# Performance work log

Hardware: AMD Instinct MI355X
Metric: run time of the kernel (lower is better)

## Reference

```python
import jax, jax.numpy as jnp
import numpy as np

V, NJ, NB, NP, NK = 6890, 24, 10, 207, 19
PARENTS = [-1,0,0,0,1,2,3,4,5,6,7,8,9,9,9,12,13,14,16,17,18,19,20,21]


def setup_inputs() -> dict:
    key = jax.random.key(0)
    ks = jax.random.split(key, 9)
    N = 2048
    return {
        "beta": jax.random.normal(ks[0], (N, NB), jnp.float32),
        "theta": jax.random.normal(ks[1], (N, NJ, 3), jnp.float32) * 0.2,
        "trans": jax.random.normal(ks[2], (N, 3), jnp.float32),
        "shapedirs": jax.random.normal(ks[3], (V, 3, NB), jnp.float32) * 0.03,
        "v_template": jax.random.normal(ks[4], (V, 3), jnp.float32),
        "J_regressor": jax.random.uniform(ks[5], (NJ, V), jnp.float32) / V,
        "posedirs": jax.random.normal(ks[6], (V, 3, NP), jnp.float32) * 0.01,
        "weights": jax.nn.softmax(jax.random.normal(ks[7], (V, NJ), jnp.float32) * 4.0, axis=-1),
        "joint_regressor": jax.random.uniform(ks[8], (V, NK), jnp.float32) / V,
    }


def rodrigues(r):
    # r: [M,3] axis-angle -> [M,3,3] rotation matrices
    theta = jnp.maximum(jnp.linalg.norm(r, axis=-1, keepdims=True),
                        jnp.finfo(r.dtype).tiny)  # [M,1]
    rh = r / theta
    c = jnp.cos(theta)[:, :, None]  # [M,1,1]
    s = jnp.sin(theta)[:, :, None]
    z = jnp.zeros_like(rh[:, 0])
    K = jnp.stack([z, -rh[:, 2], rh[:, 1],
                   rh[:, 2], z, -rh[:, 0],
                   -rh[:, 1], rh[:, 0], z], axis=1).reshape(-1, 3, 3)
    outer = rh[:, :, None] * rh[:, None, :]
    return c * jnp.eye(3, dtype=r.dtype) + (1.0 - c) * outer + s * K


def reference(beta, theta, trans, shapedirs, v_template, J_regressor, posedirs, weights, joint_regressor):
    N = beta.shape[0]
    dt = beta.dtype
    v_shaped = jnp.einsum('nb,vcb->nvc', beta, shapedirs) + v_template  # [N,V,3]
    J = jnp.einsum('jv,nvc->njc', J_regressor, v_shaped)                # [N,24,3]
    # pose rotations and pose blendshapes
    R = rodrigues(theta.reshape(-1, 3)).reshape(N, NJ, 3, 3)
    lrotmin = (R[:, 1:] - jnp.eye(3, dtype=dt)).reshape(N, NP)
    v_posed = v_shaped + jnp.einsum('np,vcp->nvc', lrotmin, posedirs)
    # kinematic chain: 24 small 4x4 transforms with parent dependencies
    bottom = jnp.broadcast_to(jnp.array([0., 0., 0., 1.], dtype=dt), (N, 1, 4))
    def make_A(Ri, t):  # [N,3,3],[N,3] -> [N,4,4]
        return jnp.concatenate([jnp.concatenate([Ri, t[:, :, None]], axis=2), bottom], axis=1)
    G = [make_A(R[:, 0], J[:, 0])]
    for i in range(1, NJ):
        p = PARENTS[i]
        G.append(G[p] @ make_A(R[:, i], J[:, i] - J[:, p]))
    G = jnp.stack(G, axis=1)  # [N,24,4,4]
    # subtract rest-pose joint contribution
    Jh = jnp.concatenate([J, jnp.zeros((N, NJ, 1), dt)], axis=2)[..., None]  # [N,24,4,1]
    corr = G @ Jh
    G_rel = G - jnp.concatenate([jnp.zeros((N, NJ, 4, 3), dt), corr], axis=3)
    # linear blend skinning
    T = jnp.einsum('njab,vj->nvab', G_rel, weights)  # [N,V,4,4]
    vh = jnp.concatenate([v_posed, jnp.ones((N, V, 1), dt)], axis=2)  # [N,V,4]
    v = jnp.einsum('nvab,nvb->nva', T, vh)[..., :3]
    verts = v + trans[:, None, :]
    joints = jnp.einsum('nvc,vk->nkc', verts, joint_regressor)  # [N,19,3]
    return verts, joints
```

## Files before the change

kernel.cpp:

```cpp
#include <hip/hip_runtime.h>

#define V      6890
#define NJ     24
#define NB     10
#define NP     207
#define NK     19
#define NBATCH 2048
#define KP     224
#define KC     217
#define VC     (V*3)
#define VCP    20736
#define BN     32
#define BV     64
#define VST4   260
#define VSEG   1723
#define KSTEPS 648
#define JSP    18
#define JCH    9

using bh8   = __attribute__((ext_vector_type(8))) short;
using u16x4 = __attribute__((ext_vector_type(4))) unsigned short;
using f32x4 = __attribute__((ext_vector_type(4))) float;

__constant__ int PAR[NJ] = {-1,0,0,0,1,2,3,4,5,6,7,8,9,9,9,12,13,14,16,17,18,19,20,21};

__device__ __forceinline__ unsigned short f2bf(float f) {
    unsigned int u = __float_as_uint(f);
    u += 0x7FFFu + ((u >> 16) & 1u);
    return (unsigned short)(u >> 16);
}
__device__ __forceinline__ float bf2f(unsigned short h) {
    return __uint_as_float((unsigned int)h << 16);
}

__global__ __launch_bounds__(256) void k_prep(const float* __restrict__ Jreg,
                                              const float* __restrict__ vtmpl,
                                              const float* __restrict__ sdirs,
                                              const float* __restrict__ pdirs,
                                              const float* __restrict__ jreg,
                                              float* __restrict__ JB,
                                              unsigned short* __restrict__ Bmat,
                                              unsigned short* __restrict__ JbigT) {
    int blk = blockIdx.x, tid = threadIdx.x;
    if (blk < 792) {
        int vs = blk & 3, og = blk >> 2;
        int o = og*4 + (tid >> 6);
        int lane = tid & 63;
        int j = o/33, t = o%33, c = t/11, m = t%11;
        int lo = vs*VSEG + lane, hi = min(V, vs*VSEG + VSEG);
        const float* jr = Jreg + j*V;
        float s = 0.f;
        if (m == 0) { for (int v = lo; v < hi; v += 64) s += jr[v] * vtmpl[v*3 + c]; }
        else        { for (int v = lo; v < hi; v += 64) s += jr[v] * sdirs[(v*3 + c)*NB + (m-1)]; }
        #pragma unroll
        for (int d = 1; d < 64; d <<= 1) s += __shfl_xor(s, d);
        if (lane == 0) atomicAdd(&JB[(j*3 + c)*11 + m], s);
    } else if (blk < 792 + 18144) {
        int gid = (blk - 792)*256 + tid;
        int vc = gid / KP, k = gid - vc*KP;
        float val;
        if (vc >= VC)     val = 0.f;
        else if (k < NB)  val = sdirs[vc*NB + k];
        else if (k < KC)  val = pdirs[vc*NP + (k - NB)];
        else if (k == KC) val = vtmpl[vc];
        else              val = 0.f;
        Bmat[((size_t)(k >> 5)*VCP + vc)*32 + (k & 31)] = f2bf(val);
    } else {
        int gid = (blk - 792 - 18144)*256 + tid;
        int kc = gid / VCP, vc = gid - kc*VCP;
        float val = 0.f;
        if (kc < NK*3 && vc < VC && (kc % 3) == (vc % 3))
            val = jreg[(vc/3)*NK + (kc/3)];
        JbigT[((size_t)(vc >> 5)*64 + kc)*32 + (vc & 31)] = f2bf(val);
    }
}

__global__ __launch_bounds__(64) void k_pern(const float* __restrict__ beta,
                                             const float* __restrict__ theta,
                                             const float* __restrict__ trans,
                                             const float* __restrict__ JB,
                                             unsigned short* __restrict__ Arow,
                                             unsigned short* __restrict__ Gt) {
    int n = blockIdx.x, tid = threadIdx.x;
    __shared__ float Rsm[NJ][9];
    __shared__ float Jsm[NJ][3];
    __shared__ float Gsm[NJ][12];

    if (tid < NJ) {
        const float* th = theta + (n*NJ + tid)*3;
        float x = th[0], y = th[1], z = th[2];
        float nrm = sqrtf(x*x + y*y + z*z);
        float t = fmaxf(nrm, 1.1754944e-38f);
        float inv = 1.0f / t;
        float rx = x*inv, ry = y*inv, rz = z*inv;
        float c = cosf(t), s = sinf(t), oc = 1.0f - c;
        Rsm[tid][0] = c + oc*rx*rx;      Rsm[tid][1] = oc*rx*ry - s*rz;  Rsm[tid][2] = oc*rx*rz + s*ry;
        Rsm[tid][3] = oc*ry*rx + s*rz;   Rsm[tid][4] = c + oc*ry*ry;     Rsm[tid][5] = oc*ry*rz - s*rx;
        Rsm[tid][6] = oc*rz*rx - s*ry;   Rsm[tid][7] = oc*rz*ry + s*rx;  Rsm[tid][8] = c + oc*rz*rz;
    } else if (tid < 2*NJ) {
        int j = tid - NJ;
        #pragma unroll
        for (int c = 0; c < 3; ++c) {
            float s = JB[(j*3+c)*11 + 0];
            #pragma unroll
            for (int b = 0; b < NB; ++b) s += JB[(j*3+c)*11 + 1 + b] * beta[n*NB + b];
            Jsm[j][c] = s;
        }
    }
    __syncthreads();

    if (tid < 12) {
        int a = tid >> 2, b = tid & 3;
        Gsm[0][a*4+b] = (b < 3) ? Rsm[0][a*3+b] : Jsm[0][a];
    }
    __syncthreads();
    for (int i = 1; i < NJ; ++i) {
        if (tid < 12) {
            int a = tid >> 2, b = tid & 3;
            int p = PAR[i];
            float acc = (b == 3) ? Gsm[p][a*4+3] : 0.0f;
            #pragma unroll
            for (int k = 0; k < 3; ++k) {
                float aval = (b < 3) ? Rsm[i][k*3+b] : (Jsm[i][k] - Jsm[p][k]);
                acc += Gsm[p][a*4+k] * aval;
            }
            Gsm[i][a*4+b] = acc;
        }
        __syncthreads();
    }
    if (tid < NJ) {
        int j = tid;
        #pragma unroll
        for (int a = 0; a < 3; ++a) {
            float t3 = Gsm[j][a*4+3]
                     - (Gsm[j][a*4+0]*Jsm[j][0] + Gsm[j][a*4+1]*Jsm[j][1] + Gsm[j][a*4+2]*Jsm[j][2])
                     + trans[n*3 + a];
            Gsm[j][a*4+3] = t3;
        }
    }
    __syncthreads();
    unsigned short* gt = Gt + n*512;
    for (int idx = tid; idx < 512; idx += 64) {
        int e = idx >> 5, j = idx & 31;
        float val = (e < 12 && j < NJ) ? Gsm[j][e] : 0.0f;
        gt[idx] = f2bf(val);
    }
    for (int k = tid; k < KP; k += 64) {
        float val;
        if (k < NB) val = beta[n*NB + k];
        else if (k < KC) {
            int p = k - NB; int jj = p/9 + 1; int rr = p%9;
            val = Rsm[jj][rr] - ((rr==0 || rr==4 || rr==8) ? 1.0f : 0.0f);
        } else if (k == KC) val = 1.0f;
        else val = 0.0f;
        Arow[((size_t)(k >> 5)*NBATCH + n)*32 + (k & 31)] = f2bf(val);
    }
}

__global__ __launch_bounds__(256, 4) void k_main(const unsigned short* __restrict__ Arow,
                                                 const unsigned short* __restrict__ Bmat,
                                                 const unsigned short* __restrict__ Gt,
                                                 const float* __restrict__ weights,
                                                 float* __restrict__ verts) {
    __shared__ __attribute__((aligned(16))) unsigned short vhsm[BN*VST4];

    int tid = threadIdx.x;
    int wv = tid >> 6, lane = tid & 63;
    int l15 = lane & 15, jg = lane >> 4;
    int nb = blockIdx.x, vb = blockIdx.y;
    int n0 = nb * BN, v0 = vb * BV, vc0 = v0 * 3;
    int vcw0 = vc0 + wv*48;

    bh8 wfrag[4];
    #pragma unroll
    for (int mt = 0; mt < 4; ++mt) {
        int vr = v0 + mt*16 + l15;
        bh8 f = {0,0,0,0,0,0,0,0};
        if (jg < 3 && vr < V) {
            const float4* wp = (const float4*)(weights + (size_t)vr*NJ + jg*8);
            float4 w0 = wp[0], w1 = wp[1];
            f[0]=(short)f2bf(w0.x); f[1]=(short)f2bf(w0.y); f[2]=(short)f2bf(w0.z); f[3]=(short)f2bf(w0.w);
            f[4]=(short)f2bf(w1.x); f[5]=(short)f2bf(w1.y); f[6]=(short)f2bf(w1.z); f[7]=(short)f2bf(w1.w);
        }
        wfrag[mt] = f;
    }

    int c4[3];
    #pragma unroll
    for (int ct = 0; ct < 3; ++ct) {
        int vcw = wv*48 + ct*16 + l15;
        c4[ct] = (vcw/3)*4 + vcw%3;
    }
    int tri = (((lane % 3)*16) + lane/3) * 4;

    const unsigned short* abase = Arow + ((size_t)n0 + l15)*32 + jg*8;
    const unsigned short* bbase = Bmat + ((size_t)vcw0 + l15)*32 + jg*8;
    f32x4 acc[2][3] = {};
    #pragma unroll
    for (int ks = 0; ks < 7; ++ks) {
        bh8 a0 = *(const bh8*)(abase + (size_t)ks*NBATCH*32);
        bh8 a1 = *(const bh8*)(abase + (size_t)ks*NBATCH*32 + 16*32);
        bh8 b0 = *(const bh8*)(bbase + (size_t)ks*VCP*32);
        bh8 b1 = *(const bh8*)(bbase + (size_t)ks*VCP*32 + 16*32);
        bh8 b2 = *(const bh8*)(bbase + (size_t)ks*VCP*32 + 32*32);
        acc[0][0] = __builtin_amdgcn_mfma_f32_16x16x32_bf16(a0, b0, acc[0][0], 0, 0, 0);
        acc[0][1] = __builtin_amdgcn_mfma_f32_16x16x32_bf16(a0, b1, acc[0][1], 0, 0, 0);
        acc[0][2] = __builtin_amdgcn_mfma_f32_16x16x32_bf16(a0, b2, acc[0][2], 0, 0, 0);
        acc[1][0] = __builtin_amdgcn_mfma_f32_16x16x32_bf16(a1, b0, acc[1][0], 0, 0, 0);
        acc[1][1] = __builtin_amdgcn_mfma_f32_16x16x32_bf16(a1, b1, acc[1][1], 0, 0, 0);
        acc[1][2] = __builtin_amdgcn_mfma_f32_16x16x32_bf16(a1, b2, acc[1][2], 0, 0, 0);
    }

    #pragma unroll
    for (int mt = 0; mt < 2; ++mt)
        #pragma unroll
        for (int ct = 0; ct < 3; ++ct)
            #pragma unroll
            for (int r = 0; r < 4; ++r)
                vhsm[(mt*16 + jg*4 + r)*VST4 + c4[ct]] = f2bf(acc[mt][ct][r]);
    __syncthreads();

    const unsigned short* gbase = Gt + ((size_t)(n0 + wv*8))*512 + l15*32 + jg*8;
    #pragma unroll
    for (int nl = 0; nl < 8; ++nl) {
        bh8 gfr = *(const bh8*)(gbase + nl*512);
        int n_loc = wv*8 + nl;
        #pragma unroll
        for (int mt = 0; mt < 4; ++mt) {
            f32x4 z = {0.f, 0.f, 0.f, 0.f};
            f32x4 t = __builtin_amdgcn_mfma_f32_16x16x32_bf16(gfr, wfrag[mt], z, 0, 0, 0);
            u16x4 vh4 = *(const u16x4*)&vhsm[n_loc*VST4 + (mt*16 + l15)*4];
            float p = t[0]*bf2f(vh4[0]) + t[1]*bf2f(vh4[1]) + t[2]*bf2f(vh4[2]) + t[3];
            float pp = __int_as_float(__builtin_amdgcn_ds_bpermute(tri, __float_as_int(p)));
            int col = vc0 + mt*48 + lane;
            if (lane < 48 && col < VC)
                verts[(size_t)(n0 + n_loc)*VC + col] = pp;
        }
    }
}

__global__ __launch_bounds__(256) void k_joints(const float* __restrict__ verts,
                                                const unsigned short* __restrict__ JbigT,
                                                float* __restrict__ jpart) {
    __shared__ __attribute__((aligned(16))) unsigned short vt[32*128];

    int tid = threadIdx.x;
    int lane = tid & 63, wv = tid >> 6;
    int l15 = lane & 15, jg = lane >> 4;
    int nt = blockIdx.x, ks = blockIdx.y;
    int n0 = nt * 32;
    int step0 = ks * (JCH*4);

    int row[4], c4[4];
    #pragma unroll
    for (int i = 0; i < 4; ++i) {
        int idx = i*256 + tid;
        row[i] = idx >> 5; c4[i] = idx & 31;
    }

    float2 rg[8];
    auto issue = [&](int ch) {
        int k0f = (step0 + ch*4) * 32;
        #pragma unroll
        for (int i = 0; i < 4; ++i) {
            const float* p = verts + (size_t)(n0 + row[i])*VC + k0f + c4[i]*4;
            rg[2*i+0] = *(const float2*)(p);
            rg[2*i+1] = *(const float2*)(p+2);
        }
    };

    issue(0);
    f32x4 acc[2] = {};
    #pragma unroll 1
    for (int ch = 0; ch < JCH; ++ch) {
        __syncthreads();
        #pragma unroll
        for (int i = 0; i < 4; ++i) {
            u16x4 w;
            w[0] = f2bf(rg[2*i].x); w[1] = f2bf(rg[2*i].y);
            w[2] = f2bf(rg[2*i+1].x); w[3] = f2bf(rg[2*i+1].y);
            int sidx = (row[i]*128 + c4[i]*4) ^ ((row[i] & 7) << 3);
            *(u16x4*)&vt[sidx] = w;
        }
        __syncthreads();
        if (ch + 1 < JCH) issue(ch + 1);
        #pragma unroll
        for (int kk = 0; kk < 4; ++kk) {
            int r0 = l15, r1 = 16 + l15;
            bh8 a0 = *(const bh8*)&vt[(r0*128 + kk*32 + jg*8) ^ ((r0 & 7) << 3)];
            bh8 a1 = *(const bh8*)&vt[(r1*128 + kk*32 + jg*8) ^ ((r1 & 7) << 3)];
            bh8 b  = *(const bh8*)(JbigT + ((size_t)(step0 + ch*4 + kk)*64 + wv*16 + l15)*32 + jg*8);
            acc[0] = __builtin_amdgcn_mfma_f32_16x16x32_bf16(a0, b, acc[0], 0, 0, 0);
            acc[1] = __builtin_amdgcn_mfma_f32_16x16x32_bf16(a1, b, acc[1], 0, 0, 0);
        }
    }
    float* jp = jpart + ((size_t)ks*NBATCH + n0)*64 + wv*16 + l15;
    #pragma unroll
    for (int mt = 0; mt < 2; ++mt)
        #pragma unroll
        for (int r = 0; r < 4; ++r)
            jp[(size_t)(mt*16 + jg*4 + r)*64] = acc[mt][r];
}

__global__ __launch_bounds__(256) void k_jred(const float* __restrict__ jpart,
                                              float* __restrict__ joints) {
    int idx = blockIdx.x*256 + threadIdx.x;
    if (idx >= NBATCH*NK*3) return;
    int n = idx / (NK*3), i = idx - n*(NK*3);
    float s = 0.f;
    #pragma unroll
    for (int ks = 0; ks < JSP; ++ks)
        s += jpart[((size_t)ks*NBATCH + n)*64 + i];
    joints[idx] = s;
}

extern "C" void kernel_launch(void* const* d_in, const int* in_sizes, int n_in,
                              void* d_out, int out_size, void* d_ws, size_t ws_size,
                              hipStream_t stream) {
    const float* beta  = (const float*)d_in[0];
    const float* theta = (const float*)d_in[1];
    const float* trans = (const float*)d_in[2];
    const float* sdirs = (const float*)d_in[3];
    const float* vtmpl = (const float*)d_in[4];
    const float* jregJ = (const float*)d_in[5];
    const float* pdirs = (const float*)d_in[6];
    const float* wgts  = (const float*)d_in[7];
    const float* jregK = (const float*)d_in[8];

    float* verts  = (float*)d_out;
    float* joints = verts + (size_t)NBATCH * VC;

    char* ws = (char*)d_ws;
    float*          JB    = (float*)ws;
    unsigned short* Arow  = (unsigned short*)(ws + 4096);
    unsigned short* Gt    = (unsigned short*)(ws + 4096 + 917504);
    unsigned short* Bmat  = (unsigned short*)(ws + 4096 + 917504 + 2097152);
    unsigned short* JbigT = (unsigned short*)(ws + 4096 + 917504 + 2097152 + 9289728);
    float*          jpart = (float*)(ws + 4096 + 917504 + 2097152 + 9289728 + 2654208);

    hipMemsetAsync(JB, 0, 4096, stream);

    k_prep <<<792 + 18144 + 5184, 256, 0, stream>>>(jregJ, vtmpl, sdirs, pdirs, jregK, JB, Bmat, JbigT);
    k_pern <<<NBATCH, 64, 0, stream>>>(beta, theta, trans, JB, Arow, Gt);
    dim3 g4(NBATCH/BN, (V + BV - 1)/BV);
    k_main <<<g4, 256, 0, stream>>>(Arow, Bmat, Gt, wgts, verts);
    dim3 g5(NBATCH/BN, JSP);
    k_joints<<<g5, 256, 0, stream>>>(verts, JbigT, jpart);
    k_jred <<<(NBATCH*NK*3 + 255)/256, 256, 0, stream>>>(jpart, joints);
}
```

Measured before the change: 161.9 us.

## Make k_main persistent over batch tiles and fuse joint reduction via atomics

k_main now launches 16 batch splits per vertex tile and loops over 4 batch tiles each. The per-tile weight fragments and index setup are reused across iterations, the G fragments are preloaded, and the shared vertex buffer is double-buffered. Separately, k_joints accumulates its partial sums straight into the joints output with atomicAdd after a memset, which removes the k_jred kernel and the jpart round trip. The cost is a much smaller grid (16x108 blocks), less parallelism to hide latency, and float atomics whose summation order is nondeterministic.

```diff
diff --git a/kernel.cpp b/kernel.cpp
--- a/kernel.cpp
+++ b/kernel.cpp
@@ -12,6 +12,8 @@
 #define VCP    20736
 #define BN     32
 #define BV     64
+#define NSPLIT 16
+#define ITERS  (NBATCH/BN/NSPLIT)
 #define VST4   260
 #define VSEG   1723
 #define KSTEPS 648
@@ -162,13 +164,13 @@
                                                  const unsigned short* __restrict__ Gt,
                                                  const float* __restrict__ weights,
                                                  float* __restrict__ verts) {
-    __shared__ __attribute__((aligned(16))) unsigned short vhsm[BN*VST4];
+    __shared__ __attribute__((aligned(16))) unsigned short vhsm[2][BN*VST4];
 
     int tid = threadIdx.x;
     int wv = tid >> 6, lane = tid & 63;
     int l15 = lane & 15, jg = lane >> 4;
-    int nb = blockIdx.x, vb = blockIdx.y;
-    int n0 = nb * BN, v0 = vb * BV, vc0 = v0 * 3;
+    int ns = blockIdx.x, vb = blockIdx.y;
+    int v0 = vb * BV, vc0 = v0 * 3;
     int vcw0 = vc0 + wv*48;
 
     bh8 wfrag[4];
@@ -192,56 +194,68 @@
         c4[ct] = (vcw/3)*4 + vcw%3;
     }
     int tri = (((lane % 3)*16) + lane/3) * 4;
-
-    const unsigned short* abase = Arow + ((size_t)n0 + l15)*32 + jg*8;
     const unsigned short* bbase = Bmat + ((size_t)vcw0 + l15)*32 + jg*8;
-    f32x4 acc[2][3] = {};
-    #pragma unroll
-    for (int ks = 0; ks < 7; ++ks) {
-        bh8 a0 = *(const bh8*)(abase + (size_t)ks*NBATCH*32);
-        bh8 a1 = *(const bh8*)(abase + (size_t)ks*NBATCH*32 + 16*32);
-        bh8 b0 = *(const bh8*)(bbase + (size_t)ks*VCP*32);
-        bh8 b1 = *(const bh8*)(bbase + (size_t)ks*VCP*32 + 16*32);
-        bh8 b2 = *(const bh8*)(bbase + (size_t)ks*VCP*32 + 32*32);
-        acc[0][0] = __builtin_amdgcn_mfma_f32_16x16x32_bf16(a0, b0, acc[0][0], 0, 0, 0);
-        acc[0][1] = __builtin_amdgcn_mfma_f32_16x16x32_bf16(a0, b1, acc[0][1], 0, 0, 0);
-        acc[0][2] = __builtin_amdgcn_mfma_f32_16x16x32_bf16(a0, b2, acc[0][2], 0, 0, 0);
-        acc[1][0] = __builtin_amdgcn_mfma_f32_16x16x32_bf16(a1, b0, acc[1][0], 0, 0, 0);
-        acc[1][1] = __builtin_amdgcn_mfma_f32_16x16x32_bf16(a1, b1, acc[1][1], 0, 0, 0);
-        acc[1][2] = __builtin_amdgcn_mfma_f32_16x16x32_bf16(a1, b2, acc[1][2], 0, 0, 0);
-    }
-
-    #pragma unroll
-    for (int mt = 0; mt < 2; ++mt)
-        #pragma unroll
-        for (int ct = 0; ct < 3; ++ct)
-            #pragma unroll
-            for (int r = 0; r < 4; ++r)
-                vhsm[(mt*16 + jg*4 + r)*VST4 + c4[ct]] = f2bf(acc[mt][ct][r]);
-    __syncthreads();
-
-    const unsigned short* gbase = Gt + ((size_t)(n0 + wv*8))*512 + l15*32 + jg*8;
-    #pragma unroll
-    for (int nl = 0; nl < 8; ++nl) {
-        bh8 gfr = *(const bh8*)(gbase + nl*512);
-        int n_loc = wv*8 + nl;
-        #pragma unroll
-        for (int mt = 0; mt < 4; ++mt) {
-            f32x4 z = {0.f, 0.f, 0.f, 0.f};
-            f32x4 t = __builtin_amdgcn_mfma_f32_16x16x32_bf16(gfr, wfrag[mt], z, 0, 0, 0);
-            u16x4 vh4 = *(const u16x4*)&vhsm[n_loc*VST4 + (mt*16 + l15)*4];
-            float p = t[0]*bf2f(vh4[0]) + t[1]*bf2f(vh4[1]) + t[2]*bf2f(vh4[2]) + t[3];
-            float pp = __int_as_float(__builtin_amdgcn_ds_bpermute(tri, __float_as_int(p)));
-            int col = vc0 + mt*48 + lane;
-            if (lane < 48 && col < VC)
-                verts[(size_t)(n0 + n_loc)*VC + col] = pp;
-        }
+
+    int cur = 0;
+    #pragma unroll 1
+    for (int it = 0; it < ITERS; ++it) {
+        int n0 = (ns*ITERS + it) * BN;
+
+        bh8 gfr[8];
+        const unsigned short* gbase = Gt + ((size_t)(n0 + wv*8))*512 + l15*32 + jg*8;
+        #pragma unroll
+        for (int nl = 0; nl < 8; ++nl)
+            gfr[nl] = *(const bh8*)(gbase + nl*512);
+
+        const unsigned short* abase = Arow + ((size_t)n0 + l15)*32 + jg*8;
+        f32x4 acc[2][3] = {};
+        #pragma unroll
+        for (int ks = 0; ks < 7; ++ks) {
+            bh8 a0 = *(const bh8*)(abase + (size_t)ks*NBATCH*32);
+            bh8 a1 = *(const bh8*)(abase + (size_t)ks*NBATCH*32 + 16*32);
+            bh8 b0 = *(const bh8*)(bbase + (size_t)ks*VCP*32);
+            bh8 b1 = *(const bh8*)(bbase + (size_t)ks*VCP*32 + 16*32);
+            bh8 b2 = *(const bh8*)(bbase + (size_t)ks*VCP*32 + 32*32);
+            acc[0][0] = __builtin_amdgcn_mfma_f32_16x16x32_bf16(a0, b0, acc[0][0], 0, 0, 0);
+            acc[0][1] = __builtin_amdgcn_mfma_f32_16x16x32_bf16(a0, b1, acc[0][1], 0, 0, 0);
+            acc[0][2] = __builtin_amdgcn_mfma_f32_16x16x32_bf16(a0, b2, acc[0][2], 0, 0, 0);
+            acc[1][0] = __builtin_amdgcn_mfma_f32_16x16x32_bf16(a1, b0, acc[1][0], 0, 0, 0);
+            acc[1][1] = __builtin_amdgcn_mfma_f32_16x16x32_bf16(a1, b1, acc[1][1], 0, 0, 0);
+            acc[1][2] = __builtin_amdgcn_mfma_f32_16x16x32_bf16(a1, b2, acc[1][2], 0, 0, 0);
+        }
+
+        unsigned short* vs = &vhsm[cur][0];
+        #pragma unroll
+        for (int mt = 0; mt < 2; ++mt)
+            #pragma unroll
+            for (int ct = 0; ct < 3; ++ct)
+                #pragma unroll
+                for (int r = 0; r < 4; ++r)
+                    vs[(mt*16 + jg*4 + r)*VST4 + c4[ct]] = f2bf(acc[mt][ct][r]);
+        __syncthreads();
+
+        #pragma unroll
+        for (int nl = 0; nl < 8; ++nl) {
+            int n_loc = wv*8 + nl;
+            #pragma unroll
+            for (int mt = 0; mt < 4; ++mt) {
+                f32x4 z = {0.f, 0.f, 0.f, 0.f};
+                f32x4 t = __builtin_amdgcn_mfma_f32_16x16x32_bf16(gfr[nl], wfrag[mt], z, 0, 0, 0);
+                u16x4 vh4 = *(const u16x4*)&vs[n_loc*VST4 + (mt*16 + l15)*4];
+                float p = t[0]*bf2f(vh4[0]) + t[1]*bf2f(vh4[1]) + t[2]*bf2f(vh4[2]) + t[3];
+                float pp = __int_as_float(__builtin_amdgcn_ds_bpermute(tri, __float_as_int(p)));
+                int col = vc0 + mt*48 + lane;
+                if (lane < 48 && col < VC)
+                    verts[(size_t)(n0 + n_loc)*VC + col] = pp;
+            }
+        }
+        cur ^= 1;
     }
 }
 
 __global__ __launch_bounds__(256) void k_joints(const float* __restrict__ verts,
                                                 const unsigned short* __restrict__ JbigT,
-                                                float* __restrict__ jpart) {
+                                                float* __restrict__ joints) {
     __shared__ __attribute__((aligned(16))) unsigned short vt[32*128];
 
     int tid = threadIdx.x;
@@ -294,24 +308,14 @@
             acc[1] = __builtin_amdgcn_mfma_f32_16x16x32_bf16(a1, b, acc[1], 0, 0, 0);
         }
     }
-    float* jp = jpart + ((size_t)ks*NBATCH + n0)*64 + wv*16 + l15;
-    #pragma unroll
-    for (int mt = 0; mt < 2; ++mt)
-        #pragma unroll
-        for (int r = 0; r < 4; ++r)
-            jp[(size_t)(mt*16 + jg*4 + r)*64] = acc[mt][r];
-}
-
-__global__ __launch_bounds__(256) void k_jred(const float* __restrict__ jpart,
-                                              float* __restrict__ joints) {
-    int idx = blockIdx.x*256 + threadIdx.x;
-    if (idx >= NBATCH*NK*3) return;
-    int n = idx / (NK*3), i = idx - n*(NK*3);
-    float s = 0.f;
-    #pragma unroll
-    for (int ks = 0; ks < JSP; ++ks)
-        s += jpart[((size_t)ks*NBATCH + n)*64 + i];
-    joints[idx] = s;
+    int kc = wv*16 + l15;
+    if (kc < NK*3) {
+        #pragma unroll
+        for (int mt = 0; mt < 2; ++mt)
+            #pragma unroll
+            for (int r = 0; r < 4; ++r)
+                atomicAdd(&joints[(size_t)(n0 + mt*16 + jg*4 + r)*(NK*3) + kc], acc[mt][r]);
+    }
 }
 
 extern "C" void kernel_launch(void* const* d_in, const int* in_sizes, int n_in,
@@ -336,15 +340,14 @@
     unsigned short* Gt    = (unsigned short*)(ws + 4096 + 917504);
     unsigned short* Bmat  = (unsigned short*)(ws + 4096 + 917504 + 2097152);
     unsigned short* JbigT = (unsigned short*)(ws + 4096 + 917504 + 2097152 + 9289728);
-    float*          jpart = (float*)(ws + 4096 + 917504 + 2097152 + 9289728 + 2654208);
 
     hipMemsetAsync(JB, 0, 4096, stream);
+    hipMemsetAsync(joints, 0, (size_t)NBATCH*NK*3*sizeof(float), stream);
 
     k_prep <<<792 + 18144 + 5184, 256, 0, stream>>>(jregJ, vtmpl, sdirs, pdirs, jregK, JB, Bmat, JbigT);
     k_pern <<<NBATCH, 64, 0, stream>>>(beta, theta, trans, JB, Arow, Gt);
-    dim3 g4(NBATCH/BN, (V + BV - 1)/BV);
+    dim3 g4(NSPLIT, (V + BV - 1)/BV);
     k_main <<<g4, 256, 0, stream>>>(Arow, Bmat, Gt, wgts, verts);
     dim3 g5(NBATCH/BN, JSP);
-    k_joints<<<g5, 256, 0, stream>>>(verts, JbigT, jpart);
-    k_jred <<<(NBATCH*NK*3 + 255)/256, 256, 0, stream>>>(jpart, joints);
-}
+    k_joints<<<g5, 256, 0, stream>>>(verts, JbigT, joints);
+}
```

New measurement: 248.9 us. 1.54x slower.

## Fuse joint regression into main skinning kernel using LDS tile and atomics

Applied to the files above, without the earlier changes.

Each main-kernel block now stores its computed vertex tile in shared memory as bf16 and immediately multiplies it by the joint regressor with MFMA, atomically accumulating partial joints into the output. This removes the separate joints kernel that re-read all vertices from global memory, and the partial-sum reduction kernel. It adds shared memory, many global atomics and an extra memset, and makes float summation order nondeterministic.

```diff
diff --git a/kernel.cpp b/kernel.cpp
--- a/kernel.cpp
+++ b/kernel.cpp
@@ -13,10 +13,8 @@
 #define BN     32
 #define BV     64
 #define VST4   260
+#define VS2    200
 #define VSEG   1723
-#define KSTEPS 648
-#define JSP    18
-#define JCH    9
 
 using bh8   = __attribute__((ext_vector_type(8))) short;
 using u16x4 = __attribute__((ext_vector_type(4))) unsigned short;
@@ -161,8 +159,11 @@
                                                  const unsigned short* __restrict__ Bmat,
                                                  const unsigned short* __restrict__ Gt,
                                                  const float* __restrict__ weights,
-                                                 float* __restrict__ verts) {
+                                                 const unsigned short* __restrict__ JbigT,
+                                                 float* __restrict__ verts,
+                                                 float* __restrict__ joints) {
     __shared__ __attribute__((aligned(16))) unsigned short vhsm[BN*VST4];
+    __shared__ __attribute__((aligned(16))) unsigned short vsm2[BN*VS2];
 
     int tid = threadIdx.x;
     int wv = tid >> 6, lane = tid & 63;
@@ -231,87 +232,34 @@
             f32x4 t = __builtin_amdgcn_mfma_f32_16x16x32_bf16(gfr, wfrag[mt], z, 0, 0, 0);
             u16x4 vh4 = *(const u16x4*)&vhsm[n_loc*VST4 + (mt*16 + l15)*4];
             float p = t[0]*bf2f(vh4[0]) + t[1]*bf2f(vh4[1]) + t[2]*bf2f(vh4[2]) + t[3];
+            if (jg < 3)
+                vsm2[n_loc*VS2 + (mt*16 + l15)*3 + jg] = f2bf(p);
             float pp = __int_as_float(__builtin_amdgcn_ds_bpermute(tri, __float_as_int(p)));
             int col = vc0 + mt*48 + lane;
             if (lane < 48 && col < VC)
                 verts[(size_t)(n0 + n_loc)*VC + col] = pp;
         }
     }
-}
-
-__global__ __launch_bounds__(256) void k_joints(const float* __restrict__ verts,
-                                                const unsigned short* __restrict__ JbigT,
-                                                float* __restrict__ jpart) {
-    __shared__ __attribute__((aligned(16))) unsigned short vt[32*128];
-
-    int tid = threadIdx.x;
-    int lane = tid & 63, wv = tid >> 6;
-    int l15 = lane & 15, jg = lane >> 4;
-    int nt = blockIdx.x, ks = blockIdx.y;
-    int n0 = nt * 32;
-    int step0 = ks * (JCH*4);
-
-    int row[4], c4[4];
-    #pragma unroll
-    for (int i = 0; i < 4; ++i) {
-        int idx = i*256 + tid;
-        row[i] = idx >> 5; c4[i] = idx & 31;
-    }
-
-    float2 rg[8];
-    auto issue = [&](int ch) {
-        int k0f = (step0 + ch*4) * 32;
-        #pragma unroll
-        for (int i = 0; i < 4; ++i) {
-            const float* p = verts + (size_t)(n0 + row[i])*VC + k0f + c4[i]*4;
-            rg[2*i+0] = *(const float2*)(p);
-            rg[2*i+1] = *(const float2*)(p+2);
-        }
-    };
-
-    issue(0);
-    f32x4 acc[2] = {};
-    #pragma unroll 1
-    for (int ch = 0; ch < JCH; ++ch) {
-        __syncthreads();
-        #pragma unroll
-        for (int i = 0; i < 4; ++i) {
-            u16x4 w;
-            w[0] = f2bf(rg[2*i].x); w[1] = f2bf(rg[2*i].y);
-            w[2] = f2bf(rg[2*i+1].x); w[3] = f2bf(rg[2*i+1].y);
-            int sidx = (row[i]*128 + c4[i]*4) ^ ((row[i] & 7) << 3);
-            *(u16x4*)&vt[sidx] = w;
-        }
-        __syncthreads();
-        if (ch + 1 < JCH) issue(ch + 1);
-        #pragma unroll
-        for (int kk = 0; kk < 4; ++kk) {
-            int r0 = l15, r1 = 16 + l15;
-            bh8 a0 = *(const bh8*)&vt[(r0*128 + kk*32 + jg*8) ^ ((r0 & 7) << 3)];
-            bh8 a1 = *(const bh8*)&vt[(r1*128 + kk*32 + jg*8) ^ ((r1 & 7) << 3)];
-            bh8 b  = *(const bh8*)(JbigT + ((size_t)(step0 + ch*4 + kk)*64 + wv*16 + l15)*32 + jg*8);
-            acc[0] = __builtin_amdgcn_mfma_f32_16x16x32_bf16(a0, b, acc[0], 0, 0, 0);
-            acc[1] = __builtin_amdgcn_mfma_f32_16x16x32_bf16(a1, b, acc[1], 0, 0, 0);
-        }
-    }
-    float* jp = jpart + ((size_t)ks*NBATCH + n0)*64 + wv*16 + l15;
-    #pragma unroll
-    for (int mt = 0; mt < 2; ++mt)
-        #pragma unroll
-        for (int r = 0; r < 4; ++r)
-            jp[(size_t)(mt*16 + jg*4 + r)*64] = acc[mt][r];
-}
-
-__global__ __launch_bounds__(256) void k_jred(const float* __restrict__ jpart,
-                                              float* __restrict__ joints) {
-    int idx = blockIdx.x*256 + threadIdx.x;
-    if (idx >= NBATCH*NK*3) return;
-    int n = idx / (NK*3), i = idx - n*(NK*3);
-    float s = 0.f;
-    #pragma unroll
-    for (int ks = 0; ks < JSP; ++ks)
-        s += jpart[((size_t)ks*NBATCH + n)*64 + i];
-    joints[idx] = s;
+    __syncthreads();
+
+    f32x4 jacc[2] = {};
+    const unsigned short* jbase = JbigT + (((size_t)(vc0 >> 5))*64 + wv*16 + l15)*32 + jg*8;
+    #pragma unroll
+    for (int ks = 0; ks < 6; ++ks) {
+        bh8 a0 = *(const bh8*)&vsm2[l15*VS2 + ks*32 + jg*8];
+        bh8 a1 = *(const bh8*)&vsm2[(16 + l15)*VS2 + ks*32 + jg*8];
+        bh8 b  = *(const bh8*)(jbase + (size_t)ks*64*32);
+        jacc[0] = __builtin_amdgcn_mfma_f32_16x16x32_bf16(a0, b, jacc[0], 0, 0, 0);
+        jacc[1] = __builtin_amdgcn_mfma_f32_16x16x32_bf16(a1, b, jacc[1], 0, 0, 0);
+    }
+    int kc = wv*16 + l15;
+    if (kc < NK*3) {
+        #pragma unroll
+        for (int mt = 0; mt < 2; ++mt)
+            #pragma unroll
+            for (int r = 0; r < 4; ++r)
+                atomicAdd(&joints[(size_t)(n0 + mt*16 + jg*4 + r)*(NK*3) + kc], jacc[mt][r]);
+    }
 }
 
 extern "C" void kernel_launch(void* const* d_in, const int* in_sizes, int n_in,
@@ -336,15 +284,12 @@
     unsigned short* Gt    = (unsigned short*)(ws + 4096 + 917504);
     unsigned short* Bmat  = (unsigned short*)(ws + 4096 + 917504 + 2097152);
     unsigned short* JbigT = (unsigned short*)(ws + 4096 + 917504 + 2097152 + 9289728);
-    float*          jpart = (float*)(ws + 4096 + 917504 + 2097152 + 9289728 + 2654208);
 
     hipMemsetAsync(JB, 0, 4096, stream);
+    hipMemsetAsync(joints, 0, (size_t)NBATCH*NK*3*sizeof(float), stream);
 
     k_prep <<<792 + 18144 + 5184, 256, 0, stream>>>(jregJ, vtmpl, sdirs, pdirs, jregK, JB, Bmat, JbigT);
     k_pern <<<NBATCH, 64, 0, stream>>>(beta, theta, trans, JB, Arow, Gt);
     dim3 g4(NBATCH/BN, (V + BV - 1)/BV);
-    k_main <<<g4, 256, 0, stream>>>(Arow, Bmat, Gt, wgts, verts);
-    dim3 g5(NBATCH/BN, JSP);
-    k_joints<<<g5, 256, 0, stream>>>(verts, JbigT, jpart);
-    k_jred <<<(NBATCH*NK*3 + 255)/256, 256, 0, stream>>>(jpart, joints);
-}
+    k_main <<<g4, 256, 0, stream>>>(Arow, Bmat, Gt, wgts, JbigT, verts, joints);
+}
```

After: 168.6 us. +4.2%, slower.

## Double-buffer B tiles in LDS via async global_load_lds and prefetch A

Applied to the files above, without the earlier changes.

Stages the block's B-matrix slice for each K-step into a double-buffered shared-memory tile using direct global-to-LDS loads, and prefetches the next step's A fragments into registers while the current step's MFMAs run. The aim is to overlap global-memory latency with matrix math instead of issuing a dependent global load before each MFMA group. In exchange it adds about 24KB of LDS per block, which may lower occupancy under the 4-blocks launch bound, and a block-wide barrier on every K-step. B rows are already contiguous per block, so there is little reuse to gain.

```diff
diff --git a/kernel.cpp b/kernel.cpp
--- a/kernel.cpp
+++ b/kernel.cpp
@@ -162,6 +162,7 @@
                                                  const unsigned short* __restrict__ Gt,
                                                  const float* __restrict__ weights,
                                                  float* __restrict__ verts) {
+    __shared__ __attribute__((aligned(16))) unsigned short Bsm[2][192*32];
     __shared__ __attribute__((aligned(16))) unsigned short vhsm[BN*VST4];
 
     int tid = threadIdx.x;
@@ -169,7 +170,6 @@
     int l15 = lane & 15, jg = lane >> 4;
     int nb = blockIdx.x, vb = blockIdx.y;
     int n0 = nb * BN, v0 = vb * BV, vc0 = v0 * 3;
-    int vcw0 = vc0 + wv*48;
 
     bh8 wfrag[4];
     #pragma unroll
@@ -193,22 +193,46 @@
     }
     int tri = (((lane % 3)*16) + lane/3) * 4;
 
+    auto stageB = [&](int buf, int ks) {
+        const unsigned short* src = Bmat + ((size_t)ks*VCP + vc0)*32;
+        #pragma unroll
+        for (int i = 0; i < 3; ++i) {
+            int u = (wv*3 + i)*64;
+            __builtin_amdgcn_global_load_lds(
+                (const __attribute__((address_space(1))) void*)(src + (size_t)(u + lane)*8),
+                (__attribute__((address_space(3))) void*)(&Bsm[buf][0] + (size_t)u*8),
+                16, 0, 0);
+        }
+    };
+
     const unsigned short* abase = Arow + ((size_t)n0 + l15)*32 + jg*8;
-    const unsigned short* bbase = Bmat + ((size_t)vcw0 + l15)*32 + jg*8;
+    stageB(0, 0);
+    bh8 a0 = *(const bh8*)(abase);
+    bh8 a1 = *(const bh8*)(abase + 16*32);
+    __syncthreads();
+
     f32x4 acc[2][3] = {};
     #pragma unroll
     for (int ks = 0; ks < 7; ++ks) {
-        bh8 a0 = *(const bh8*)(abase + (size_t)ks*NBATCH*32);
-        bh8 a1 = *(const bh8*)(abase + (size_t)ks*NBATCH*32 + 16*32);
-        bh8 b0 = *(const bh8*)(bbase + (size_t)ks*VCP*32);
-        bh8 b1 = *(const bh8*)(bbase + (size_t)ks*VCP*32 + 16*32);
-        bh8 b2 = *(const bh8*)(bbase + (size_t)ks*VCP*32 + 32*32);
+        int cur = ks & 1;
+        bh8 a0n = a0, a1n = a1;
+        if (ks < 6) {
+            stageB(cur ^ 1, ks + 1);
+            a0n = *(const bh8*)(abase + (size_t)(ks+1)*NBATCH*32);
+            a1n = *(const bh8*)(abase + (size_t)(ks+1)*NBATCH*32 + 16*32);
+        }
+        const unsigned short* bs = &Bsm[cur][0];
+        bh8 b0 = *(const bh8*)&bs[(size_t)(wv*48 +  0 + l15)*32 + jg*8];
+        bh8 b1 = *(const bh8*)&bs[(size_t)(wv*48 + 16 + l15)*32 + jg*8];
+        bh8 b2 = *(const bh8*)&bs[(size_t)(wv*48 + 32 + l15)*32 + jg*8];
         acc[0][0] = __builtin_amdgcn_mfma_f32_16x16x32_bf16(a0, b0, acc[0][0], 0, 0, 0);
         acc[0][1] = __builtin_amdgcn_mfma_f32_16x16x32_bf16(a0, b1, acc[0][1], 0, 0, 0);
         acc[0][2] = __builtin_amdgcn_mfma_f32_16x16x32_bf16(a0, b2, acc[0][2], 0, 0, 0);
         acc[1][0] = __builtin_amdgcn_mfma_f32_16x16x32_bf16(a1, b0, acc[1][0], 0, 0, 0);
         acc[1][1] = __builtin_amdgcn_mfma_f32_16x16x32_bf16(a1, b1, acc[1][1], 0, 0, 0);
         acc[1][2] = __builtin_amdgcn_mfma_f32_16x16x32_bf16(a1, b2, acc[1][2], 0, 0, 0);
+        if (ks < 6) __syncthreads();
+        a0 = a0n; a1 = a1n;
     }
 
     #pragma unroll
```

Result: slower. 174.9 us (+8.0%).
